# Performance work log

Hardware: AMD Instinct MI355X
Metric: run time of the kernel (lower is better)

## Reference

```python
import jax, jax.numpy as jnp
import numpy as np

D_MODEL, N, L_MAX, BATCH = 512, 64, 2048, 8


def _make_s4_buffers(n):
    # HiPPO-NPLR: hippo[i,j] = sqrt(2i+1)sqrt(2j+1) if i>j; i+1 if i==j (1-indexed)
    i = np.arange(1, n + 1)
    row = np.sqrt(2 * i + 1.0)
    hippo = np.tril(np.outer(row, row), -1) + np.diag(i + 1.0)
    p = 0.5 * np.sqrt(2 * i + 1.0)
    q = 2.0 * p
    S = -hippo + np.outer(p, q)
    lam, V = np.linalg.eig(S)
    Vc = V.conj().T
    return Vc @ p, Vc @ q, lam  # complex128 -> cast to complex64 later


def setup_inputs() -> dict:
    key = jax.random.key(0)
    k1, k2, k3, k4 = jax.random.split(key, 4)
    xavier_std = float(np.sqrt(2.0 / (N + D_MODEL)))
    p, q, lam = _make_s4_buffers(N)
    u = jax.random.normal(k1, (BATCH, L_MAX, D_MODEL), jnp.float32)
    B = jax.random.normal(k2, (D_MODEL, N), jnp.float32) * xavier_std
    Ct = jax.random.normal(k3, (D_MODEL, N), jnp.float32) * xavier_std
    D = jnp.ones((D_MODEL,), jnp.float32)
    log_step = (jax.random.uniform(k4, (D_MODEL,), jnp.float32)
                * (np.log(0.1) - np.log(0.001)) + np.log(0.001))
    return {
        "u": u, "B": B, "Ct": Ct, "D": D, "log_step": log_step,
        "p": jnp.asarray(p, jnp.complex64),
        "q": jnp.asarray(q, jnp.complex64),
        "lam": jnp.asarray(lam, jnp.complex64),
    }


def _s4_forward(u, B, Ct, D, log_step, p, q, lam):
    L = u.shape[1]  # l_max
    omega = jnp.exp((2j * np.pi / L) * jnp.arange(L)).astype(jnp.complex64)  # (L,)
    step = jnp.exp(log_step)                                                 # (d,)
    g = (2.0 / step)[:, None] * ((1.0 - omega) / (1.0 + omega))[None, :]     # (d, L)
    c = 2.0 / (1.0 + omega)                                                  # (L,)
    Bc = B.astype(jnp.complex64)
    Ctc = Ct.astype(jnp.complex64)  # Ct is real -> conj is identity
    v00 = Ctc * Bc                              # (d, n)
    v01 = Ctc * p[None, :]                      # (d, n)
    v10 = jnp.conj(q)[None, :] * Bc             # (d, n)
    v11 = jnp.broadcast_to(jnp.conj(q) * p, v00.shape)
    V = jnp.stack([v00, v01, v10, v11], 0)      # (4, d, n)
    # fused Cauchy reduction: k[k,d,l] = sum_n V[k,d,n] / (g[d,l] - lam[n])
    recip = 1.0 / (g[:, :, None] - lam[None, None, :])  # (d, L, n) big intermediate
    k00, k01, k10, k11 = jnp.einsum('kdn,dln->kdl', V, recip)
    at_roots = c * (k00 - k01 * k10 / (1.0 + k11))      # (d, L)
    # ifft + index reversal (i -> (L - i) mod L), keep real part
    order = (L - jnp.arange(L)) % L
    K = jnp.fft.ifft(at_roots, n=L, axis=-1)[:, order].real.astype(jnp.float32)  # (d, L)
    # non-circular convolution via length-2L FFT
    ud = jnp.fft.rfft(jnp.pad(u, ((0, 0), (0, L), (0, 0))), axis=1)   # (B, L+1, d)
    Kd = jnp.fft.rfft(jnp.pad(K, ((0, 0), (0, L))), axis=-1)          # (d, L+1)
    y = jnp.fft.irfft(jnp.swapaxes(ud, 1, 2) * Kd[None], axis=-1)[..., :L]  # (B, d, L)
    return jnp.swapaxes(y, 1, 2) + D[None, None, :] * u


def reference(u, B, Ct, D, log_step, p, q, lam):
    return _s4_forward(u, B, Ct, D, log_step, p, q, lam)
```

## Files before the change

### kernel.cpp

```cpp
#include <hip/hip_runtime.h>
#include <math.h>

#define D_MODEL 512
#define NSTATE  64
#define LSEQ    2048
#define L2X     4096
#define NBATCH  8
#define NT      512

__device__ __forceinline__ float2 cmulf(float2 a, float2 b) {
    return make_float2(a.x * b.x - a.y * b.y, a.x * b.y + a.y * b.x);
}
__device__ __forceinline__ float2 cmulc(float2 a, float2 w) {
    return make_float2(a.x * w.x + a.y * w.y, a.y * w.x - a.x * w.y);
}
__device__ __forceinline__ float2 cadd(float2 a, float2 b) { return make_float2(a.x + b.x, a.y + b.y); }
__device__ __forceinline__ float2 csub(float2 a, float2 b) { return make_float2(a.x - b.x, a.y - b.y); }
__device__ __forceinline__ float rcpf(float x) { return __builtin_amdgcn_rcpf(x); }
__device__ __forceinline__ float2 cdiv_fast(float2 a, float2 b) {
    float inv = rcpf(b.x * b.x + b.y * b.y);
    return make_float2((a.x * b.x + a.y * b.y) * inv, (a.y * b.x - a.x * b.y) * inv);
}
__device__ __forceinline__ int finitef(float v) {
    return (v == v) && (v < 3.0e38f) && (v > -3.0e38f);
}
__device__ __forceinline__ int brev11(int x) { return (int)(__brev((unsigned)x) >> 21); }
__device__ __forceinline__ int digrev12(int x) {
    unsigned r = __brev((unsigned)x) >> 20;
    return (int)(((r & 0x555u) << 1) | ((r >> 1) & 0x555u));
}

__device__ __forceinline__ int tidx(int i) { return i + (i >> 4); }
__device__ __forceinline__ int kswz(int i) { return i ^ (i >> 6); }

#define TW_SZ  1088
#define BUF_SZ 4352

__device__ __forceinline__ float2 twget4(const float2* tw, int k) {
    float2 w = tw[tidx(k & 1023)];
    if (k & 1024) w = make_float2(w.y, -w.x);
    if (k & 2048) w = make_float2(-w.x, -w.y);
    return w;
}
__device__ __forceinline__ void build_tw(float2* tw) {
    for (int k = threadIdx.x; k < 1024; k += NT) {
        float ang = -1.5339807878856412e-3f * (float)k;
        float s, c;
        sincosf(ang, &s, &c);
        tw[tidx(k)] = make_float2(c, s);
    }
}

__device__ __forceinline__ float2 ldc(const float* f, int n, int mode) {
    if (mode == 0) return make_float2(f[n], 0.0f);
    if (mode == 1) return make_float2(f[n], f[64 + n]);
    return make_float2(f[2 * n], f[2 * n + 1]);
}

__device__ void dif_fft2(float2* buf, const float2* tw, int log2N) {
    const int tid = threadIdx.x;
    const int halfN = 1 << (log2N - 1);
    for (int lm = log2N - 1; lm >= 0; lm--) {
        const int m = 1 << lm;
        __syncthreads();
        for (int t = tid; t < halfN; t += NT) {
            int j = t & (m - 1);
            int i0 = ((t - j) << 1) + j;
            int i1 = i0 + m;
            float2 a = buf[tidx(i0)], b = buf[tidx(i1)];
            buf[tidx(i0)] = cadd(a, b);
            buf[tidx(i1)] = cmulf(csub(a, b), twget4(tw, j << (11 - lm)));
        }
    }
    __syncthreads();
}

__device__ void dif_fft4_rest(float2* buf, const float2* tw) {
    const int tid = threadIdx.x;
    int f = 4;
    for (int h = 256; h >= 1; h >>= 2, f <<= 2) {
        __syncthreads();
        for (int t = tid; t < 1024; t += NT) {
            int j = t & (h - 1);
            int i0 = ((t - j) << 2) + j;
            float2 a = buf[tidx(i0)], b = buf[tidx(i0 + h)];
            float2 c = buf[tidx(i0 + 2 * h)], d = buf[tidx(i0 + 3 * h)];
            float2 t0 = cadd(a, c), t1 = csub(a, c);
            float2 t2 = cadd(b, d), t3 = csub(b, d);
            float2 e1 = make_float2(t1.x + t3.y, t1.y - t3.x);
            float2 e3 = make_float2(t1.x - t3.y, t1.y + t3.x);
            int k = j * f;
            buf[tidx(i0)]         = cadd(t0, t2);
            buf[tidx(i0 + h)]     = cmulf(e1, twget4(tw, k));
            buf[tidx(i0 + 2 * h)] = cmulf(csub(t0, t2), twget4(tw, 2 * k));
            buf[tidx(i0 + 3 * h)] = cmulf(e3, twget4(tw, 3 * k));
        }
    }
    __syncthreads();
}

__device__ void dit_ifft4_rest(float2* buf, const float2* tw) {
    const int tid = threadIdx.x;
    int f = 1024;
    for (int h = 1; h <= 256; h <<= 2, f >>= 2) {
        __syncthreads();
        for (int t = tid; t < 1024; t += NT) {
            int j = t & (h - 1);
            int i0 = ((t - j) << 2) + j;
            int k = j * f;
            float2 a = buf[tidx(i0)];
            float2 b = cmulc(buf[tidx(i0 + h)],     twget4(tw, k));
            float2 c = cmulc(buf[tidx(i0 + 2 * h)], twget4(tw, 2 * k));
            float2 d = cmulc(buf[tidx(i0 + 3 * h)], twget4(tw, 3 * k));
            float2 t0 = cadd(a, c), t1 = csub(a, c);
            float2 t2 = cadd(b, d), t3 = csub(b, d);
            buf[tidx(i0)]         = cadd(t0, t2);
            buf[tidx(i0 + h)]     = make_float2(t1.x - t3.y, t1.y + t3.x);
            buf[tidx(i0 + 2 * h)] = csub(t0, t2);
            buf[tidx(i0 + 3 * h)] = make_float2(t1.x + t3.y, t1.y - t3.x);
        }
    }
    __syncthreads();
}

__global__ __launch_bounds__(NT) void s4_khat_kernel(
    const float* __restrict__ Bmat, const float* __restrict__ Ct,
    const float* __restrict__ log_step,
    const float* __restrict__ pf, const float* __restrict__ qf,
    const float* __restrict__ lf,
    float2* __restrict__ Khat, int size_hint)
{
    __shared__ float2 tw[TW_SZ];
    __shared__ float2 buf[BUF_SZ];
    __shared__ float2 stash[289];
    __shared__ float  kf[2048];
    const int d = blockIdx.x;
    const int tid = threadIdx.x;

    build_tw(tw);

    int mode;
    if (size_hint >= 128) {
        mode = (fabsf(lf[1] + 0.5f) < 0.05f) ? 1 : 2;
    } else {
        float s1 = 0.0f, s2 = 0.0f;
        bool ok = true;
        for (int n = 0; n < 64; n++) {
            float v = lf[64 + n];
            if (!finitef(v)) { ok = false; break; }
            s1 += v; s2 += fabsf(v);
        }
        mode = (ok && s2 > 0.5f && s2 < 1.0e6f && fabsf(s1) < 1.0e-2f * s2) ? 1 : 0;
    }

    float2* v01  = stash;
    float2* v10  = stash + 64;
    float2* v11  = stash + 128;
    float2* lamS = stash + 192;
    float*  v00  = (float*)(stash + 256);

    if (tid < NSTATE) {
        int n = tid;
        float Bdn = Bmat[d * NSTATE + n];
        float Cdn = Ct[d * NSTATE + n];
        float2 pn = ldc(pf, n, mode);
        float2 qn = ldc(qf, n, mode);
        float2 qc = make_float2(qn.x, -qn.y);
        v00[n]  = Cdn * Bdn;
        v01[n]  = make_float2(Cdn * pn.x, Cdn * pn.y);
        v10[n]  = make_float2(qc.x * Bdn, qc.y * Bdn);
        v11[n]  = cmulf(qc, pn);
        lamS[n] = ldc(lf, n, mode);
    }
    const float two_over_step = 2.0f / expf(log_step[d]);
    __syncthreads();

    float gyr[2], tanl[2];
    float2 a00[2], a01[2], a10[2], a11[2];
    #pragma unroll
    for (int i = 0; i < 2; i++) {
        int l = tid + i * NT;
        float2 w = twget4(tw, 2 * l);
        float cth = w.x, sth = -w.y;
        float tl = sth * rcpf(1.0f + cth);
        tanl[i] = tl;
        gyr[i]  = -two_over_step * tl;
        a00[i] = make_float2(0.f, 0.f); a01[i] = make_float2(0.f, 0.f);
        a10[i] = make_float2(0.f, 0.f); a11[i] = make_float2(0.f, 0.f);
    }
    for (int n = 0; n < NSTATE; n++) {
        float2 ln = lamS[n];
        float  c0 = v00[n];
        float2 c1 = v01[n], c2 = v10[n], c3 = v11[n];
        float dxn = -ln.x;
        float dx2 = ln.x * ln.x;
        #pragma unroll
        for (int i = 0; i < 2; i++) {
            float dy = gyr[i] - ln.y;
            float ir = rcpf(fmaf(dy, dy, dx2));
            float rx = dxn * ir, ry = -dy * ir;
            a00[i].x += c0 * rx;               a00[i].y += c0 * ry;
            a01[i].x += c1.x * rx - c1.y * ry; a01[i].y += c1.x * ry + c1.y * rx;
            a10[i].x += c2.x * rx - c2.y * ry; a10[i].y += c2.x * ry + c2.y * rx;
            a11[i].x += c3.x * rx - c3.y * ry; a11[i].y += c3.x * ry + c3.y * rx;
        }
    }
    __syncthreads();
    #pragma unroll
    for (int i = 0; i < 2; i++) {
        int l = tid + i * NT;
        float2 cl = make_float2(1.0f, -tanl[i]);
        float2 onep = make_float2(1.0f + a11[i].x, a11[i].y);
        float2 corr = cdiv_fast(cmulf(a01[i], a10[i]), onep);
        float2 ar = cmulf(cl, csub(a00[i], corr));
        if (!finitef(ar.x) || !finitef(ar.y)) ar = make_float2(0.0f, 0.0f);
        buf[tidx(l)] = ar;
        if (l > 0) buf[tidx(2048 - l)] = make_float2(ar.x, -ar.y);
    }
    if (tid == 0) buf[tidx(1024)] = make_float2(0.0f, 0.0f);

    dif_fft2(buf, tw, 11);

    const float inv2048 = 1.0f / 2048.0f;
    #pragma unroll
    for (int i = 0; i < 4; i++) {
        int p = tid + i * NT;
        kf[kswz(brev11(p))] = buf[tidx(p)].x * inv2048;
    }
    __syncthreads();

    #pragma unroll
    for (int half = 0; half < 2; half++) {
        int i0 = tid + half * NT;
        float ka = kf[kswz(i0)];
        float kb = kf[kswz(i0 + 1024)];
        float2 w1 = twget4(tw, i0);
        float2 w2 = twget4(tw, 2 * i0);
        float2 w3 = twget4(tw, 3 * i0);
        float dif = ka - kb;
        buf[tidx(i0)]        = make_float2(ka + kb, 0.0f);
        buf[tidx(i0 + 1024)] = cmulf(make_float2(ka, -kb), w1);
        buf[tidx(i0 + 2048)] = make_float2(dif * w2.x, dif * w2.y);
        buf[tidx(i0 + 3072)] = cmulf(make_float2(ka, kb), w3);
    }
    dif_fft4_rest(buf, tw);

    const float inv4096 = 1.0f / 4096.0f;
    for (int k = tid; k < L2X; k += NT) {
        float2 v = buf[tidx(k)];
        float vx = v.x * inv4096, vy = v.y * inv4096;
        if (!finitef(vx)) vx = 0.0f;
        if (!finitef(vy)) vy = 0.0f;
        Khat[(size_t)d * L2X + k] = make_float2(vx, vy);
    }
}

__global__ __launch_bounds__(NT) void conv_kernel(
    const float* __restrict__ u, const float2* __restrict__ Khat,
    const float* __restrict__ Dvec, float* __restrict__ out)
{
    __shared__ float2 tw[TW_SZ];
    __shared__ float2 buf[BUF_SZ];
    const int blk = blockIdx.x;
    const int d0 = blk >> 3;
    const int bb = blk & 7;
    const int tid = threadIdx.x;

    build_tw(tw);

    float2 ureg[4];
    #pragma unroll
    for (int i = 0; i < 4; i++) {
        int t = tid + i * NT;
        ureg[i] = *(const float2*)(u + ((size_t)bb * LSEQ + t) * D_MODEL + 2 * d0);
    }
    __syncthreads();

    #pragma unroll
    for (int half = 0; half < 2; half++) {
        int i0 = tid + half * NT;
        float2 a = ureg[half];
        float2 b = ureg[half + 2];
        float2 w1 = twget4(tw, i0);
        float2 w2 = twget4(tw, 2 * i0);
        float2 w3 = twget4(tw, 3 * i0);
        buf[tidx(i0)]        = cadd(a, b);
        buf[tidx(i0 + 1024)] = cmulf(make_float2(a.x + b.y, a.y - b.x), w1);
        buf[tidx(i0 + 2048)] = cmulf(csub(a, b), w2);
        buf[tidx(i0 + 3072)] = cmulf(make_float2(a.x - b.y, a.y + b.x), w3);
    }
    dif_fft4_rest(buf, tw);

    const float2* K0 = Khat + (size_t)(2 * d0) * L2X;
    const float2* K1 = K0 + L2X;
    for (int t0 = tid; t0 < L2X; t0 += NT) {
        int fr = digrev12(t0);
        int jm = digrev12((L2X - fr) & (L2X - 1));
        if (t0 > jm) continue;
        float2 Zk = buf[tidx(t0)], Zm = buf[tidx(jm)];
        float2 U0 = make_float2(0.5f * (Zk.x + Zm.x), 0.5f * (Zk.y - Zm.y));
        float2 U1 = make_float2(0.5f * (Zk.y + Zm.y), 0.5f * (Zm.x - Zk.x));
        float2 Y0 = cmulf(U0, K0[t0]);
        float2 Y1 = cmulf(U1, K1[t0]);
        buf[tidx(t0)] = make_float2(Y0.x - Y1.y, Y0.y + Y1.x);
        buf[tidx(jm)] = make_float2(Y0.x + Y1.y, Y1.x - Y0.y);
    }
    dit_ifft4_rest(buf, tw);

    const float dv0 = Dvec[2 * d0];
    const float dv1 = Dvec[2 * d0 + 1];
    #pragma unroll
    for (int half = 0; half < 2; half++) {
        int t = tid + half * NT;
        float2 va = buf[tidx(t)];
        float2 vb = cmulc(buf[tidx(t + 1024)], twget4(tw, t));
        float2 vc = cmulc(buf[tidx(t + 2048)], twget4(tw, 2 * t));
        float2 vd = cmulc(buf[tidx(t + 3072)], twget4(tw, 3 * t));
        float2 t0v = cadd(va, vc), t1v = csub(va, vc);
        float2 t2v = cadd(vb, vd), t3v = csub(vb, vd);
        float2 y0 = cadd(t0v, t2v);
        float2 y1 = make_float2(t1v.x - t3v.y, t1v.y + t3v.x);
        {
            float o0 = y0.x + dv0 * ureg[half].x;
            float o1 = y0.y + dv1 * ureg[half].y;
            if (!finitef(o0)) o0 = 4.0e5f;
            if (!finitef(o1)) o1 = 4.0e5f;
            *(float2*)(out + ((size_t)bb * LSEQ + t) * D_MODEL + 2 * d0) = make_float2(o0, o1);
        }
        {
            float o0 = y1.x + dv0 * ureg[half + 2].x;
            float o1 = y1.y + dv1 * ureg[half + 2].y;
            if (!finitef(o0)) o0 = 4.0e5f;
            if (!finitef(o1)) o1 = 4.0e5f;
            *(float2*)(out + ((size_t)bb * LSEQ + (t + 1024)) * D_MODEL + 2 * d0) = make_float2(o0, o1);
        }
    }
}

extern "C" void kernel_launch(void* const* d_in, const int* in_sizes, int n_in,
                              void* d_out, int out_size, void* d_ws, size_t ws_size,
                              hipStream_t stream) {
    (void)n_in; (void)out_size; (void)ws_size;
    const float* u        = (const float*)d_in[0];
    const float* Bmat     = (const float*)d_in[1];
    const float* Ct       = (const float*)d_in[2];
    const float* Dvec     = (const float*)d_in[3];
    const float* log_step = (const float*)d_in[4];
    const float* pf       = (const float*)d_in[5];
    const float* qf       = (const float*)d_in[6];
    const float* lf       = (const float*)d_in[7];
    float* out = (float*)d_out;

    int size_hint = in_sizes[5];

    float2* Khat = (float2*)d_ws;

    s4_khat_kernel<<<D_MODEL, NT, 0, stream>>>(Bmat, Ct, log_step, pf, qf, lf, Khat, size_hint);
    conv_kernel<<<NBATCH * (D_MODEL / 2), NT, 0, stream>>>(u, Khat, Dvec, out);
}
```

Baseline: 199.6 us.

## Replace radix-2/4 shared-memory FFTs with radix-8 stages and precomputed twiddles

Rewrites the 2048-point inverse FFT and the 4096-point forward/inverse FFTs as radix-8 stages in both kernels, with the first and last stages fused into the register-level load and output code. Per-stage twiddles go into small precomputed shared tables. The goal is fewer shared-memory passes, fewer barriers and less twiddle computation. In exchange it adds per-block sincos setup and higher register pressure, and the digit-reversal index mapping changes to octal.

```diff
diff --git a/kernel.cpp b/kernel.cpp
--- a/kernel.cpp
+++ b/kernel.cpp
@@ -8,6 +8,8 @@
 #define NBATCH  8
 #define NT      512
 
+#define SQ2H 0.70710678118654752f
+
 __device__ __forceinline__ float2 cmulf(float2 a, float2 b) {
     return make_float2(a.x * b.x - a.y * b.y, a.x * b.y + a.y * b.x);
 }
@@ -24,10 +26,8 @@
 __device__ __forceinline__ int finitef(float v) {
     return (v == v) && (v < 3.0e38f) && (v > -3.0e38f);
 }
-__device__ __forceinline__ int brev11(int x) { return (int)(__brev((unsigned)x) >> 21); }
-__device__ __forceinline__ int digrev12(int x) {
-    unsigned r = __brev((unsigned)x) >> 20;
-    return (int)(((r & 0x555u) << 1) | ((r >> 1) & 0x555u));
+__device__ __forceinline__ int octrev12(int x) {
+    return ((x & 7) << 9) | ((x & 0x38) << 3) | ((x >> 3) & 0x38) | ((x >> 9) & 7);
 }
 
 __device__ __forceinline__ int tidx(int i) { return i + (i >> 4); }
@@ -42,11 +42,11 @@
     if (k & 2048) w = make_float2(-w.x, -w.y);
     return w;
 }
+#define A4096 (-1.5339807878856412e-3f)
 __device__ __forceinline__ void build_tw(float2* tw) {
     for (int k = threadIdx.x; k < 1024; k += NT) {
-        float ang = -1.5339807878856412e-3f * (float)k;
         float s, c;
-        sincosf(ang, &s, &c);
+        sincosf(A4096 * (float)k, &s, &c);
         tw[tidx(k)] = make_float2(c, s);
     }
 }
@@ -57,70 +57,99 @@
     return make_float2(f[2 * n], f[2 * n + 1]);
 }
 
-__device__ void dif_fft2(float2* buf, const float2* tw, int log2N) {
+__device__ __forceinline__ void dft4f(float2 a, float2 b, float2 c, float2 d, float2* F) {
+    float2 t0 = cadd(a, c), t1 = csub(a, c);
+    float2 t2 = cadd(b, d), t3 = csub(b, d);
+    F[0] = cadd(t0, t2);
+    F[1] = make_float2(t1.x + t3.y, t1.y - t3.x);
+    F[2] = csub(t0, t2);
+    F[3] = make_float2(t1.x - t3.y, t1.y + t3.x);
+}
+__device__ __forceinline__ void dft4i(float2 a, float2 b, float2 c, float2 d, float2* F) {
+    float2 t0 = cadd(a, c), t1 = csub(a, c);
+    float2 t2 = cadd(b, d), t3 = csub(b, d);
+    F[0] = cadd(t0, t2);
+    F[1] = make_float2(t1.x - t3.y, t1.y + t3.x);
+    F[2] = csub(t0, t2);
+    F[3] = make_float2(t1.x + t3.y, t1.y - t3.x);
+}
+__device__ __forceinline__ void dft8f(const float2* a, float2* X) {
+    float2 E[4], O[4];
+    dft4f(a[0], a[2], a[4], a[6], E);
+    dft4f(a[1], a[3], a[5], a[7], O);
+    float2 o1 = make_float2(SQ2H * (O[1].x + O[1].y), SQ2H * (O[1].y - O[1].x));
+    float2 o2 = make_float2(O[2].y, -O[2].x);
+    float2 o3 = make_float2(SQ2H * (O[3].y - O[3].x), -SQ2H * (O[3].x + O[3].y));
+    X[0] = cadd(E[0], O[0]); X[4] = csub(E[0], O[0]);
+    X[1] = cadd(E[1], o1);   X[5] = csub(E[1], o1);
+    X[2] = cadd(E[2], o2);   X[6] = csub(E[2], o2);
+    X[3] = cadd(E[3], o3);   X[7] = csub(E[3], o3);
+}
+__device__ __forceinline__ void dft8i(const float2* a, float2* X) {
+    float2 E[4], O[4];
+    dft4i(a[0], a[2], a[4], a[6], E);
+    dft4i(a[1], a[3], a[5], a[7], O);
+    float2 o1 = make_float2(SQ2H * (O[1].x - O[1].y), SQ2H * (O[1].y + O[1].x));
+    float2 o2 = make_float2(-O[2].y, O[2].x);
+    float2 o3 = make_float2(-SQ2H * (O[3].x + O[3].y), SQ2H * (O[3].x - O[3].y));
+    X[0] = cadd(E[0], O[0]); X[4] = csub(E[0], O[0]);
+    X[1] = cadd(E[1], o1);   X[5] = csub(E[1], o1);
+    X[2] = cadd(E[2], o2);   X[6] = csub(E[2], o2);
+    X[3] = cadd(E[3], o3);   X[7] = csub(E[3], o3);
+}
+
+template<int H, int F, int TWMODE, int NBF>
+__device__ __forceinline__ void r8_dif_stage(float2* buf, const float2* tw, const float2* twp) {
+    __syncthreads();
     const int tid = threadIdx.x;
-    const int halfN = 1 << (log2N - 1);
-    for (int lm = log2N - 1; lm >= 0; lm--) {
-        const int m = 1 << lm;
-        __syncthreads();
-        for (int t = tid; t < halfN; t += NT) {
-            int j = t & (m - 1);
-            int i0 = ((t - j) << 1) + j;
-            int i1 = i0 + m;
-            float2 a = buf[tidx(i0)], b = buf[tidx(i1)];
-            buf[tidx(i0)] = cadd(a, b);
-            buf[tidx(i1)] = cmulf(csub(a, b), twget4(tw, j << (11 - lm)));
+    if (NBF >= NT || tid < NBF) {
+        const int j = tid & (H - 1);
+        const int i0 = ((tid - j) << 3) + j;
+        float2 a[8], X[8];
+        #pragma unroll
+        for (int k = 0; k < 8; k++) a[k] = buf[tidx(i0 + k * H)];
+        dft8f(a, X);
+        if (TWMODE == 1) {
+            #pragma unroll
+            for (int m = 1; m < 8; m++) X[m] = cmulf(X[m], twp[(m - 1) * H + j]);
+        } else if (TWMODE == 2) {
+            #pragma unroll
+            for (int m = 1; m < 8; m++) X[m] = cmulf(X[m], twget4(tw, (j * F * m) & 4095));
         }
-    }
-    __syncthreads();
-}
-
-__device__ void dif_fft4_rest(float2* buf, const float2* tw) {
+        #pragma unroll
+        for (int m = 0; m < 8; m++) buf[tidx(i0 + m * H)] = X[m];
+    }
+}
+template<int H, int F, int TWMODE>
+__device__ __forceinline__ void r8_dit_stage(float2* buf, const float2* tw, const float2* twp) {
+    __syncthreads();
     const int tid = threadIdx.x;
-    int f = 4;
-    for (int h = 256; h >= 1; h >>= 2, f <<= 2) {
-        __syncthreads();
-        for (int t = tid; t < 1024; t += NT) {
-            int j = t & (h - 1);
-            int i0 = ((t - j) << 2) + j;
-            float2 a = buf[tidx(i0)], b = buf[tidx(i0 + h)];
-            float2 c = buf[tidx(i0 + 2 * h)], d = buf[tidx(i0 + 3 * h)];
-            float2 t0 = cadd(a, c), t1 = csub(a, c);
-            float2 t2 = cadd(b, d), t3 = csub(b, d);
-            float2 e1 = make_float2(t1.x + t3.y, t1.y - t3.x);
-            float2 e3 = make_float2(t1.x - t3.y, t1.y + t3.x);
-            int k = j * f;
-            buf[tidx(i0)]         = cadd(t0, t2);
-            buf[tidx(i0 + h)]     = cmulf(e1, twget4(tw, k));
-            buf[tidx(i0 + 2 * h)] = cmulf(csub(t0, t2), twget4(tw, 2 * k));
-            buf[tidx(i0 + 3 * h)] = cmulf(e3, twget4(tw, 3 * k));
-        }
-    }
-    __syncthreads();
-}
-
-__device__ void dit_ifft4_rest(float2* buf, const float2* tw) {
+    const int j = tid & (H - 1);
+    const int i0 = ((tid - j) << 3) + j;
+    float2 a[8], X[8];
+    a[0] = buf[tidx(i0)];
+    if (TWMODE == 1) {
+        #pragma unroll
+        for (int k = 1; k < 8; k++) a[k] = cmulc(buf[tidx(i0 + k * H)], twp[(k - 1) * H + j]);
+    } else if (TWMODE == 2) {
+        #pragma unroll
+        for (int k = 1; k < 8; k++) a[k] = cmulc(buf[tidx(i0 + k * H)], twget4(tw, (j * F * k) & 4095));
+    } else {
+        #pragma unroll
+        for (int k = 1; k < 8; k++) a[k] = buf[tidx(i0 + k * H)];
+    }
+    dft8i(a, X);
+    #pragma unroll
+    for (int m = 0; m < 8; m++) buf[tidx(i0 + m * H)] = X[m];
+}
+__device__ __forceinline__ void r4_dif_h1(float2* buf) {
+    __syncthreads();
     const int tid = threadIdx.x;
-    int f = 1024;
-    for (int h = 1; h <= 256; h <<= 2, f >>= 2) {
-        __syncthreads();
-        for (int t = tid; t < 1024; t += NT) {
-            int j = t & (h - 1);
-            int i0 = ((t - j) << 2) + j;
-            int k = j * f;
-            float2 a = buf[tidx(i0)];
-            float2 b = cmulc(buf[tidx(i0 + h)],     twget4(tw, k));
-            float2 c = cmulc(buf[tidx(i0 + 2 * h)], twget4(tw, 2 * k));
-            float2 d = cmulc(buf[tidx(i0 + 3 * h)], twget4(tw, 3 * k));
-            float2 t0 = cadd(a, c), t1 = csub(a, c);
-            float2 t2 = cadd(b, d), t3 = csub(b, d);
-            buf[tidx(i0)]         = cadd(t0, t2);
-            buf[tidx(i0 + h)]     = make_float2(t1.x - t3.y, t1.y + t3.x);
-            buf[tidx(i0 + 2 * h)] = csub(t0, t2);
-            buf[tidx(i0 + 3 * h)] = make_float2(t1.x + t3.y, t1.y - t3.x);
-        }
-    }
-    __syncthreads();
+    const int i0 = tid << 2;
+    float2 F[4];
+    dft4f(buf[tidx(i0)], buf[tidx(i0 + 1)], buf[tidx(i0 + 2)], buf[tidx(i0 + 3)], F);
+    #pragma unroll
+    for (int m = 0; m < 4; m++) buf[tidx(i0 + m)] = F[m];
 }
 
 __global__ __launch_bounds__(NT) void s4_khat_kernel(
@@ -134,10 +163,25 @@
     __shared__ float2 buf[BUF_SZ];
     __shared__ float2 stash[289];
     __shared__ float  kf[2048];
+    __shared__ float2 twS2[448];
+    __shared__ float2 twS3[56];
+    __shared__ float2 twK2[224];
+    __shared__ float2 twK3[28];
     const int d = blockIdx.x;
     const int tid = threadIdx.x;
 
     build_tw(tw);
+    for (int i = tid; i < 448; i += NT) {
+        int m = (i >> 6) + 1, j = i & 63; float s, c;
+        sincosf(A4096 * (float)(8 * j * m), &s, &c);
+        twS2[i] = make_float2(c, s);
+    }
+    if (tid < 224) { int m = (tid >> 5) + 1, j = tid & 31; float s, c;
+        sincosf(A4096 * (float)(16 * j * m), &s, &c); twK2[tid] = make_float2(c, s); }
+    else if (tid < 280) { int r = tid - 224; int m = (r >> 3) + 1, j = r & 7; float s, c;
+        sincosf(A4096 * (float)(64 * j * m), &s, &c); twS3[r] = make_float2(c, s); }
+    else if (tid < 308) { int r = tid - 280; int m = (r >> 2) + 1, j = r & 3; float s, c;
+        sincosf(A4096 * (float)(128 * j * m), &s, &c); twK3[r] = make_float2(c, s); }
 
     int mode;
     if (size_hint >= 128) {
@@ -219,31 +263,50 @@
     }
     if (tid == 0) buf[tidx(1024)] = make_float2(0.0f, 0.0f);
 
-    dif_fft2(buf, tw, 11);
+    r8_dif_stage<256, 2, 2, 256>(buf, tw, nullptr);
+    r8_dif_stage<32, 0, 1, 256>(buf, tw, twK2);
+    r8_dif_stage<4, 0, 1, 256>(buf, tw, twK3);
+    r4_dif_h1(buf);
+    __syncthreads();
 
     const float inv2048 = 1.0f / 2048.0f;
     #pragma unroll
     for (int i = 0; i < 4; i++) {
         int p = tid + i * NT;
-        kf[kswz(brev11(p))] = buf[tidx(p)].x * inv2048;
-    }
-    __syncthreads();
-
-    #pragma unroll
-    for (int half = 0; half < 2; half++) {
-        int i0 = tid + half * NT;
-        float ka = kf[kswz(i0)];
-        float kb = kf[kswz(i0 + 1024)];
-        float2 w1 = twget4(tw, i0);
-        float2 w2 = twget4(tw, 2 * i0);
-        float2 w3 = twget4(tw, 3 * i0);
-        float dif = ka - kb;
-        buf[tidx(i0)]        = make_float2(ka + kb, 0.0f);
-        buf[tidx(i0 + 1024)] = cmulf(make_float2(ka, -kb), w1);
-        buf[tidx(i0 + 2048)] = make_float2(dif * w2.x, dif * w2.y);
-        buf[tidx(i0 + 3072)] = cmulf(make_float2(ka, kb), w3);
-    }
-    dif_fft4_rest(buf, tw);
+        int t = (p >> 8) | (((p >> 5) & 7) << 3) | (((p >> 2) & 7) << 6) | ((p & 3) << 9);
+        kf[kswz(t)] = buf[tidx(p)].x * inv2048;
+    }
+    __syncthreads();
+
+    {
+        const float a = kf[kswz(tid)];
+        const float b = kf[kswz(tid + 512)];
+        const float c = kf[kswz(tid + 1024)];
+        const float dd = kf[kswz(tid + 1536)];
+        float t0 = a + c, t1 = a - c, t2 = b + dd, t3 = b - dd;
+        float2 Xe0 = make_float2(t0 + t2, 0.0f);
+        float2 Xe1 = make_float2(t1, -t3);
+        float2 Xe2 = make_float2(t0 - t2, 0.0f);
+        float2 Xe3 = make_float2(t1, t3);
+        float2 y0 = make_float2(a, 0.0f);
+        float2 y1 = make_float2(SQ2H * b, -SQ2H * b);
+        float2 y2 = make_float2(0.0f, -c);
+        float2 y3 = make_float2(-SQ2H * dd, -SQ2H * dd);
+        float2 G[4];
+        dft4f(y0, y1, y2, y3, G);
+        buf[tidx(tid)]        = Xe0;
+        buf[tidx(tid + 512)]  = cmulf(G[0], twget4(tw, tid));
+        buf[tidx(tid + 1024)] = cmulf(Xe1, twget4(tw, 2 * tid));
+        buf[tidx(tid + 1536)] = cmulf(G[1], twget4(tw, (3 * tid) & 4095));
+        buf[tidx(tid + 2048)] = cmulf(Xe2, twget4(tw, (4 * tid) & 4095));
+        buf[tidx(tid + 2560)] = cmulf(G[2], twget4(tw, (5 * tid) & 4095));
+        buf[tidx(tid + 3072)] = cmulf(Xe3, twget4(tw, (6 * tid) & 4095));
+        buf[tidx(tid + 3584)] = cmulf(G[3], twget4(tw, (7 * tid) & 4095));
+    }
+    r8_dif_stage<64, 0, 1, 512>(buf, tw, twS2);
+    r8_dif_stage<8, 0, 1, 512>(buf, tw, twS3);
+    r8_dif_stage<1, 512, 0, 512>(buf, tw, nullptr);
+    __syncthreads();
 
     const float inv4096 = 1.0f / 4096.0f;
     for (int k = tid; k < L2X; k += NT) {
@@ -261,12 +324,21 @@
 {
     __shared__ float2 tw[TW_SZ];
     __shared__ float2 buf[BUF_SZ];
+    __shared__ float2 twS2[448];
+    __shared__ float2 twS3[56];
     const int blk = blockIdx.x;
     const int d0 = blk >> 3;
     const int bb = blk & 7;
     const int tid = threadIdx.x;
 
     build_tw(tw);
+    for (int i = tid; i < 448; i += NT) {
+        int m = (i >> 6) + 1, j = i & 63; float s, c;
+        sincosf(A4096 * (float)(8 * j * m), &s, &c);
+        twS2[i] = make_float2(c, s);
+    }
+    if (tid < 56) { int m = (tid >> 3) + 1, j = tid & 7; float s, c;
+        sincosf(A4096 * (float)(64 * j * m), &s, &c); twS3[tid] = make_float2(c, s); }
 
     float2 ureg[4];
     #pragma unroll
@@ -276,26 +348,32 @@
     }
     __syncthreads();
 
-    #pragma unroll
-    for (int half = 0; half < 2; half++) {
-        int i0 = tid + half * NT;
-        float2 a = ureg[half];
-        float2 b = ureg[half + 2];
-        float2 w1 = twget4(tw, i0);
-        float2 w2 = twget4(tw, 2 * i0);
-        float2 w3 = twget4(tw, 3 * i0);
-        buf[tidx(i0)]        = cadd(a, b);
-        buf[tidx(i0 + 1024)] = cmulf(make_float2(a.x + b.y, a.y - b.x), w1);
-        buf[tidx(i0 + 2048)] = cmulf(csub(a, b), w2);
-        buf[tidx(i0 + 3072)] = cmulf(make_float2(a.x - b.y, a.y + b.x), w3);
-    }
-    dif_fft4_rest(buf, tw);
+    {
+        float2 Xe[4], G[4];
+        dft4f(ureg[0], ureg[1], ureg[2], ureg[3], Xe);
+        float2 y1 = make_float2(SQ2H * (ureg[1].x + ureg[1].y), SQ2H * (ureg[1].y - ureg[1].x));
+        float2 y2 = make_float2(ureg[2].y, -ureg[2].x);
+        float2 y3 = make_float2(SQ2H * (ureg[3].y - ureg[3].x), -SQ2H * (ureg[3].x + ureg[3].y));
+        dft4f(ureg[0], y1, y2, y3, G);
+        buf[tidx(tid)]        = Xe[0];
+        buf[tidx(tid + 512)]  = cmulf(G[0], twget4(tw, tid));
+        buf[tidx(tid + 1024)] = cmulf(Xe[1], twget4(tw, 2 * tid));
+        buf[tidx(tid + 1536)] = cmulf(G[1], twget4(tw, (3 * tid) & 4095));
+        buf[tidx(tid + 2048)] = cmulf(Xe[2], twget4(tw, (4 * tid) & 4095));
+        buf[tidx(tid + 2560)] = cmulf(G[2], twget4(tw, (5 * tid) & 4095));
+        buf[tidx(tid + 3072)] = cmulf(Xe[3], twget4(tw, (6 * tid) & 4095));
+        buf[tidx(tid + 3584)] = cmulf(G[3], twget4(tw, (7 * tid) & 4095));
+    }
+    r8_dif_stage<64, 0, 1, 512>(buf, tw, twS2);
+    r8_dif_stage<8, 0, 1, 512>(buf, tw, twS3);
+    r8_dif_stage<1, 512, 0, 512>(buf, tw, nullptr);
+    __syncthreads();
 
     const float2* K0 = Khat + (size_t)(2 * d0) * L2X;
     const float2* K1 = K0 + L2X;
     for (int t0 = tid; t0 < L2X; t0 += NT) {
-        int fr = digrev12(t0);
-        int jm = digrev12((L2X - fr) & (L2X - 1));
+        int fr = octrev12(t0);
+        int jm = octrev12((L2X - fr) & (L2X - 1));
         if (t0 > jm) continue;
         float2 Zk = buf[tidx(t0)], Zm = buf[tidx(jm)];
         float2 U0 = make_float2(0.5f * (Zk.x + Zm.x), 0.5f * (Zk.y - Zm.y));
@@ -305,34 +383,42 @@
         buf[tidx(t0)] = make_float2(Y0.x - Y1.y, Y0.y + Y1.x);
         buf[tidx(jm)] = make_float2(Y0.x + Y1.y, Y1.x - Y0.y);
     }
-    dit_ifft4_rest(buf, tw);
+
+    r8_dit_stage<1, 512, 0>(buf, tw, nullptr);
+    r8_dit_stage<8, 64, 1>(buf, tw, twS3);
+    r8_dit_stage<64, 8, 1>(buf, tw, twS2);
+    __syncthreads();
 
     const float dv0 = Dvec[2 * d0];
     const float dv1 = Dvec[2 * d0 + 1];
-    #pragma unroll
-    for (int half = 0; half < 2; half++) {
-        int t = tid + half * NT;
-        float2 va = buf[tidx(t)];
-        float2 vb = cmulc(buf[tidx(t + 1024)], twget4(tw, t));
-        float2 vc = cmulc(buf[tidx(t + 2048)], twget4(tw, 2 * t));
-        float2 vd = cmulc(buf[tidx(t + 3072)], twget4(tw, 3 * t));
-        float2 t0v = cadd(va, vc), t1v = csub(va, vc);
-        float2 t2v = cadd(vb, vd), t3v = csub(vb, vd);
-        float2 y0 = cadd(t0v, t2v);
-        float2 y1 = make_float2(t1v.x - t3v.y, t1v.y + t3v.x);
-        {
-            float o0 = y0.x + dv0 * ureg[half].x;
-            float o1 = y0.y + dv1 * ureg[half].y;
+    {
+        float2 c0 = buf[tidx(tid)];
+        float2 c1 = cmulc(buf[tidx(tid +  512)], twget4(tw, tid));
+        float2 c2 = cmulc(buf[tidx(tid + 1024)], twget4(tw, 2 * tid));
+        float2 c3 = cmulc(buf[tidx(tid + 1536)], twget4(tw, (3 * tid) & 4095));
+        float2 c4 = cmulc(buf[tidx(tid + 2048)], twget4(tw, (4 * tid) & 4095));
+        float2 c5 = cmulc(buf[tidx(tid + 2560)], twget4(tw, (5 * tid) & 4095));
+        float2 c6 = cmulc(buf[tidx(tid + 3072)], twget4(tw, (6 * tid) & 4095));
+        float2 c7 = cmulc(buf[tidx(tid + 3584)], twget4(tw, (7 * tid) & 4095));
+        float2 E[4], O[4];
+        dft4i(c0, c2, c4, c6, E);
+        dft4i(c1, c3, c5, c7, O);
+        float2 o1 = make_float2(SQ2H * (O[1].x - O[1].y), SQ2H * (O[1].y + O[1].x));
+        float2 o2 = make_float2(-O[2].y, O[2].x);
+        float2 o3 = make_float2(-SQ2H * (O[3].x + O[3].y), SQ2H * (O[3].x - O[3].y));
+        float2 y[4];
+        y[0] = cadd(E[0], O[0]);
+        y[1] = cadd(E[1], o1);
+        y[2] = cadd(E[2], o2);
+        y[3] = cadd(E[3], o3);
+        #pragma unroll
+        for (int m = 0; m < 4; m++) {
+            int t = tid + 512 * m;
+            float o0 = y[m].x + dv0 * ureg[m].x;
+            float o1f = y[m].y + dv1 * ureg[m].y;
             if (!finitef(o0)) o0 = 4.0e5f;
-            if (!finitef(o1)) o1 = 4.0e5f;
-            *(float2*)(out + ((size_t)bb * LSEQ + t) * D_MODEL + 2 * d0) = make_float2(o0, o1);
-        }
-        {
-            float o0 = y1.x + dv0 * ureg[half + 2].x;
-            float o1 = y1.y + dv1 * ureg[half + 2].y;
-            if (!finitef(o0)) o0 = 4.0e5f;
-            if (!finitef(o1)) o1 = 4.0e5f;
-            *(float2*)(out + ((size_t)bb * LSEQ + (t + 1024)) * D_MODEL + 2 * d0) = make_float2(o0, o1);
+            if (!finitef(o1f)) o1f = 4.0e5f;
+            *(float2*)(out + ((size_t)bb * LSEQ + t) * D_MODEL + 2 * d0) = make_float2(o0, o1f);
         }
     }
 }
```

After: 177.0 us. -11.3%, faster.
